# Kernel tuning notes

Measured on AMD Instinct MI355X. Metric: run time of the kernel, lower is better.

The kernel has to match this reference:

```python
import jax, jax.numpy as jnp
import numpy as np

B, T, C = 4, 2048, 1024
HEAD = 2048

def setup_inputs() -> dict:
    key = jax.random.key(0)
    ks = jax.random.split(key, 7)
    s = 1.0 / np.sqrt(C)
    return {
        "x":  jax.random.normal(ks[0], (B, T, C), dtype=jnp.float32),
        "Wq": jax.random.uniform(ks[1], (C, HEAD), dtype=jnp.float32, minval=-s, maxval=s),
        "bq": jax.random.uniform(ks[2], (HEAD,), dtype=jnp.float32, minval=-s, maxval=s),
        "Wk": jax.random.uniform(ks[3], (C, HEAD), dtype=jnp.float32, minval=-s, maxval=s),
        "bk": jax.random.uniform(ks[4], (HEAD,), dtype=jnp.float32, minval=-s, maxval=s),
        "Wv": jax.random.uniform(ks[5], (C, HEAD), dtype=jnp.float32, minval=-s, maxval=s),
        "bv": jax.random.uniform(ks[6], (HEAD,), dtype=jnp.float32, minval=-s, maxval=s),
    }

def reference(x, Wq, bq, Wk, bk, Wv, bv):
    # q,k,v: [B,T,HEAD]
    q = jnp.einsum('btc,ch->bth', x, Wq) + bq
    k = jnp.einsum('btc,ch->bth', x, Wk) + bk
    v = jnp.einsum('btc,ch->bth', x, Wv) + bv
    scale = x.shape[-1] ** -0.5  # NOTE: original scales by n_embed**-0.5, not head_size
    wei = jnp.einsum('bth,bsh->bts', q, k) * scale  # [B,T,T]
    Tn = x.shape[1]
    causal = jnp.tril(jnp.ones((Tn, Tn), dtype=bool))
    wei = jnp.where(causal, wei, -jnp.inf)
    wei = jax.nn.softmax(wei, axis=-1)
    # dropout is identity in eval mode
    out = jnp.einsum('bts,bsh->bth', wei, v)  # [B,T,HEAD]
    return out
```

## Files before the change

### kernel.cpp

```cpp
#include <hip/hip_runtime.h>


#define T_    2048
#define C_    1024
#define B_    4
#define NQK   4096
#define SCALE 0.03125f

typedef __attribute__((ext_vector_type(4))) float floatx4;
typedef __attribute__((ext_vector_type(8))) short short8;
typedef __attribute__((ext_vector_type(8))) unsigned short ushortx8;

__device__ __forceinline__ unsigned short f2bf(float f) {
  unsigned int u = __float_as_uint(f);
  unsigned int r = (u + 0x7fffu + ((u >> 16) & 1u)) >> 16;
  return (unsigned short)r;
}

__global__ void cast_x_kernel(const float* __restrict__ x, ushort* __restrict__ xbf) {
  int i = blockIdx.x * 256 + threadIdx.x;
  float4 v = ((const float4*)x)[i];
  ushort4 o;
  o.x = f2bf(v.x); o.y = f2bf(v.y); o.z = f2bf(v.z); o.w = f2bf(v.w);
  ((ushort4*)xbf)[i] = o;
}

__global__ void wcast_t_kernel(const float* __restrict__ Wq, const float* __restrict__ Wk,
                               const float* __restrict__ Wv, ushort* __restrict__ WtT) {
  int k0 = blockIdx.x * 32;
  int n0 = blockIdx.y * 32;
  const float* W = (n0 < 2048) ? Wq : (n0 < 4096 ? Wk : Wv);
  int nl0 = n0 & 2047;
  __shared__ ushort tile[32][33];
  int tx = threadIdx.x, ty = threadIdx.y;
  for (int r = ty; r < 32; r += 8)
    tile[r][tx] = f2bf(W[(size_t)(k0 + r) * 2048 + nl0 + tx]);
  __syncthreads();
  for (int r = ty; r < 32; r += 8)
    WtT[(size_t)(n0 + r) * 1024 + k0 + tx] = tile[tx][r];
}

__global__ void bias_cat_kernel(const float* __restrict__ bq, const float* __restrict__ bk,
                                const float* __restrict__ bv, float* __restrict__ bcat) {
  int i = blockIdx.x * 256 + threadIdx.x;
  if (i < 6144) {
    const float* s = (i < 2048) ? bq : (i < 4096 ? bk : bv);
    bcat[i] = s[i & 2047];
  }
}

__device__ __forceinline__ void stage128x32(const ushort* g, int ld, char* lds,
                                            int wave, int lane) {
#pragma unroll
  for (int c = 0; c < 2; ++c) {
    int chunk = wave + 4 * c;
    const ushort* gaddr = g + (size_t)(chunk * 16 + (lane >> 2)) * ld + (lane & 3) * 8;
    char* laddr = lds + chunk * 1024;
    __builtin_amdgcn_global_load_lds((const __attribute__((address_space(1))) unsigned int*)gaddr,
                                     (__attribute__((address_space(3))) unsigned int*)laddr,
                                     16, 0, 0);
  }
}

__device__ __forceinline__ void gemm_core(const ushort* A, int lda,
                                          const ushort* Bm, int ldb, int ksteps,
                                          char* ldsA, char* ldsB, floatx4 acc[4][4]) {
  int tid = threadIdx.x;
  int wave = tid >> 6, lane = tid & 63;
  int wm = wave >> 1, wn = wave & 1;
  int koff2 = ((lane >> 4) * 8) * 2;
  int rbase = lane & 15;
  for (int s = 0; s < ksteps; ++s) {
    __syncthreads();
    stage128x32(A + s * 32, lda, ldsA, wave, lane);
    stage128x32(Bm + s * 32, ldb, ldsB, wave, lane);
    __syncthreads();
    short8 af[4], bf[4];
#pragma unroll
    for (int i = 0; i < 4; ++i) {
      af[i] = *(const short8*)(ldsA + (wm * 64 + i * 16 + rbase) * 64 + koff2);
      bf[i] = *(const short8*)(ldsB + (wn * 64 + i * 16 + rbase) * 64 + koff2);
    }
#pragma unroll
    for (int i = 0; i < 4; ++i)
#pragma unroll
      for (int j = 0; j < 4; ++j)
        acc[i][j] = __builtin_amdgcn_mfma_f32_16x16x32_bf16(af[i], bf[j], acc[i][j], 0, 0, 0);
  }
}


#define MFMA16(a, b, c) __builtin_amdgcn_mfma_f32_16x16x32_bf16((a), (b), (c), 0, 0, 0)

#define GLDS16(gsrc, ldst)                                                                       \
  __builtin_amdgcn_global_load_lds((const __attribute__((address_space(1))) unsigned int*)(gsrc), \
                                   (__attribute__((address_space(3))) unsigned int*)(ldst), 16, 0, 0)

template <int LD>
__device__ __forceinline__ void stage_half(const ushort* gsrc, char* ldst) {
  GLDS16(gsrc, ldst);
  GLDS16(gsrc + 8 * LD, ldst + 1024);
}

#define BARX() do {                                        \
  __builtin_amdgcn_sched_barrier(0);                       \
  __builtin_amdgcn_s_barrier();                            \
  __builtin_amdgcn_sched_barrier(0);                       \
} while (0)

template <int LDA, int LDB>
__device__ __forceinline__ void prologue256(const ushort* Ap, const ushort* Bp,
                                            char* lds, int wave, int srcOffA, int srcOffB) {
  stage_half<LDA>(Ap + srcOffA,                     lds + wave * 2048);
  stage_half<LDA>(Ap + 128 * LDA + srcOffA,         lds + 16384 + wave * 2048);
  stage_half<LDB>(Bp + srcOffB,                     lds + 65536 + wave * 2048);
  stage_half<LDB>(Bp + 128 * LDB + srcOffB,         lds + 81920 + wave * 2048);
  stage_half<LDB>(Bp + 64 + srcOffB,                lds + 98304 + wave * 2048);
  stage_half<LDB>(Bp + 64 + 128 * LDB + srcOffB,    lds + 114688 + wave * 2048);
  __builtin_amdgcn_sched_barrier(0);
  asm volatile("s_waitcnt vmcnt(4)" ::: "memory");
  BARX();
}

template <int LDA, int LDB, bool TAIL>
__device__ __forceinline__ void iter256(const ushort* __restrict__ Ap,
                                        const ushort* __restrict__ Bp,
                                        char* lds, int kt0, int wave, int wm, int wn,
                                        int srcOffA, int srcOffB, int lnoff0,
                                        floatx4 (&acc)[8][4]) {
  char* rA0 = lds + wm * 16384;
  char* rA1 = rA0 + 32768;
  char* rB0 = lds + 65536 + (wn >> 1) * 16384 + (wn & 1) * 8192;
  char* rB1 = rB0 + 32768;
  const ushort* sA1 = Ap + (kt0 + 1) * 64 + srcOffA;
  const ushort* sA2 = Ap + (kt0 + 2) * 64 + srcOffA;
  const ushort* sB2 = Bp + (kt0 + 2) * 64 + srcOffB;
  const ushort* sB3 = Bp + (kt0 + 3) * 64 + srcOffB;
  const int lnoff1 = lnoff0 ^ 64;
  short8 af[4][2], b4[4][2];

#pragma unroll
  for (int mi = 0; mi < 4; ++mi) {
    af[mi][0] = *(const short8*)(rA0 + mi * 2048 + lnoff0);
    af[mi][1] = *(const short8*)(rA0 + mi * 2048 + lnoff1);
  }
#pragma unroll
  for (int nj = 0; nj < 4; ++nj) {
    b4[nj][0] = *(const short8*)(rB0 + nj * 2048 + lnoff0);
    b4[nj][1] = *(const short8*)(rB0 + nj * 2048 + lnoff1);
  }
  stage_half<LDA>(sA1, lds + 32768 + wave * 2048);
  stage_half<LDA>(sA1 + 128 * LDA, lds + 49152 + wave * 2048);
  __builtin_amdgcn_s_setprio(1);
#pragma unroll
  for (int mi = 0; mi < 4; ++mi)
#pragma unroll
    for (int nj = 0; nj < 4; ++nj) {
      acc[mi][nj] = MFMA16(af[mi][0], b4[nj][0], acc[mi][nj]);
      acc[mi][nj] = MFMA16(af[mi][1], b4[nj][1], acc[mi][nj]);
    }
  __builtin_amdgcn_s_setprio(0);
  BARX();

#pragma unroll
  for (int mi = 0; mi < 4; ++mi) {
    af[mi][0] = *(const short8*)(rA0 + (4 + mi) * 2048 + lnoff0);
    af[mi][1] = *(const short8*)(rA0 + (4 + mi) * 2048 + lnoff1);
  }
  if constexpr (!TAIL) {
    stage_half<LDB>(sB2, lds + 65536 + wave * 2048);
    stage_half<LDB>(sB2 + 128 * LDB, lds + 81920 + wave * 2048);
  }
  __builtin_amdgcn_s_setprio(1);
#pragma unroll
  for (int mi = 0; mi < 4; ++mi)
#pragma unroll
    for (int nj = 0; nj < 4; ++nj) {
      acc[4 + mi][nj] = MFMA16(af[mi][0], b4[nj][0], acc[4 + mi][nj]);
      acc[4 + mi][nj] = MFMA16(af[mi][1], b4[nj][1], acc[4 + mi][nj]);
    }
  __builtin_amdgcn_s_setprio(0);
  __builtin_amdgcn_sched_barrier(0);
  if constexpr (TAIL) asm volatile("s_waitcnt vmcnt(0)" ::: "memory");
  else                asm volatile("s_waitcnt vmcnt(4)" ::: "memory");
  BARX();

#pragma unroll
  for (int mi = 0; mi < 4; ++mi) {
    af[mi][0] = *(const short8*)(rA1 + mi * 2048 + lnoff0);
    af[mi][1] = *(const short8*)(rA1 + mi * 2048 + lnoff1);
  }
#pragma unroll
  for (int nj = 0; nj < 4; ++nj) {
    b4[nj][0] = *(const short8*)(rB1 + nj * 2048 + lnoff0);
    b4[nj][1] = *(const short8*)(rB1 + nj * 2048 + lnoff1);
  }
  if constexpr (!TAIL) {
    stage_half<LDA>(sA2, lds + wave * 2048);
    stage_half<LDA>(sA2 + 128 * LDA, lds + 16384 + wave * 2048);
  }
  __builtin_amdgcn_s_setprio(1);
#pragma unroll
  for (int mi = 0; mi < 4; ++mi)
#pragma unroll
    for (int nj = 0; nj < 4; ++nj) {
      acc[mi][nj] = MFMA16(af[mi][0], b4[nj][0], acc[mi][nj]);
      acc[mi][nj] = MFMA16(af[mi][1], b4[nj][1], acc[mi][nj]);
    }
  __builtin_amdgcn_s_setprio(0);
  BARX();

#pragma unroll
  for (int mi = 0; mi < 4; ++mi) {
    af[mi][0] = *(const short8*)(rA1 + (4 + mi) * 2048 + lnoff0);
    af[mi][1] = *(const short8*)(rA1 + (4 + mi) * 2048 + lnoff1);
  }
  if constexpr (!TAIL) {
    stage_half<LDB>(sB3, lds + 98304 + wave * 2048);
    stage_half<LDB>(sB3 + 128 * LDB, lds + 114688 + wave * 2048);
  }
  __builtin_amdgcn_s_setprio(1);
#pragma unroll
  for (int mi = 0; mi < 4; ++mi)
#pragma unroll
    for (int nj = 0; nj < 4; ++nj) {
      acc[4 + mi][nj] = MFMA16(af[mi][0], b4[nj][0], acc[4 + mi][nj]);
      acc[4 + mi][nj] = MFMA16(af[mi][1], b4[nj][1], acc[4 + mi][nj]);
    }
  __builtin_amdgcn_s_setprio(0);
  __builtin_amdgcn_sched_barrier(0);
  if constexpr (!TAIL) asm volatile("s_waitcnt vmcnt(4)" ::: "memory");
  BARX();
}

struct Addr256 {
  int wave, wm, wn, ln, ln15, lnoff0;
};
__device__ __forceinline__ Addr256 addr256() {
  Addr256 a;
  int tid = threadIdx.x;
  a.wave = tid >> 6; a.ln = tid & 63;
  a.wm = a.wave >> 2; a.wn = a.wave & 3;
  a.ln15 = a.ln & 15;
  a.lnoff0 = a.ln15 * 128 + (((a.ln >> 4) * 16) ^ ((a.ln15 & 7) << 4));
  return a;
}
template <int LD>
__device__ __forceinline__ int srcOff256(int wave, int ln) {
  return (wave * 16 + (ln >> 3)) * LD + (((ln & 7) * 8) ^ ((ln >> 3) << 3));
}

__global__ __launch_bounds__(512) void gemm_qk256(const ushort* __restrict__ xbf,
                                                  const ushort* __restrict__ WtT,
                                                  const float* __restrict__ bcat,
                                                  ushort* __restrict__ QK) {
  __shared__ __align__(16) char lds[131072];
  int tm = blockIdx.x, tn = blockIdx.y;
  Addr256 a = addr256();
  int srcOff = srcOff256<1024>(a.wave, a.ln);
  const ushort* Ap = xbf + (size_t)tm * 256 * 1024;
  const ushort* Bp = WtT + (size_t)tn * 256 * 1024;
  floatx4 acc[8][4];
#pragma unroll
  for (int i = 0; i < 8; ++i)
#pragma unroll
    for (int j = 0; j < 4; ++j) acc[i][j] = (floatx4){0.f, 0.f, 0.f, 0.f};

  prologue256<1024, 1024>(Ap, Bp, lds, a.wave, srcOff, srcOff);
#pragma unroll 1
  for (int i = 0; i < 7; ++i)
    iter256<1024, 1024, false>(Ap, Bp, lds, 2 * i, a.wave, a.wm, a.wn, srcOff, srcOff, a.lnoff0, acc);
  iter256<1024, 1024, true>(Ap, Bp, lds, 14, a.wave, a.wm, a.wn, srcOff, srcOff, a.lnoff0, acc);

  int colb = a.ln15, rowq = (a.ln >> 4) * 4;
  int colbase = tn * 256 + a.wn * 64 + colb;
  float bias[4];
#pragma unroll
  for (int nj = 0; nj < 4; ++nj) bias[nj] = bcat[colbase + nj * 16];
#pragma unroll
  for (int mi = 0; mi < 8; ++mi) {
    int row = tm * 256 + a.wm * 128 + mi * 16 + rowq;
#pragma unroll
    for (int r = 0; r < 4; ++r) {
      ushort* qrow = QK + (size_t)(row + r) * NQK;
#pragma unroll
      for (int nj = 0; nj < 4; ++nj)
        qrow[colbase + nj * 16] = f2bf(acc[mi][nj][r] + bias[nj]);
    }
  }
}

__global__ __launch_bounds__(512) void gemm_s256(const ushort* __restrict__ QK,
                                                 float* __restrict__ S) {
  int l = blockIdx.x, b = blockIdx.y;
  int tm = (int)((sqrtf(8.f * l + 1.f) - 1.f) * 0.5f);
  while ((tm + 1) * (tm + 2) / 2 <= l) ++tm;
  while (tm * (tm + 1) / 2 > l) --tm;
  int tn = l - tm * (tm + 1) / 2;
  __shared__ __align__(16) char lds[131072];
  Addr256 a = addr256();
  int srcOff = srcOff256<NQK>(a.wave, a.ln);
  const ushort* Ap = QK + (size_t)b * T_ * NQK + (size_t)tm * 256 * NQK;
  const ushort* Bp = QK + (size_t)b * T_ * NQK + (size_t)tn * 256 * NQK + 2048;
  floatx4 acc[8][4];
#pragma unroll
  for (int i = 0; i < 8; ++i)
#pragma unroll
    for (int j = 0; j < 4; ++j) acc[i][j] = (floatx4){0.f, 0.f, 0.f, 0.f};

  prologue256<NQK, NQK>(Ap, Bp, lds, a.wave, srcOff, srcOff);
#pragma unroll 1
  for (int i = 0; i < 15; ++i)
    iter256<NQK, NQK, false>(Ap, Bp, lds, 2 * i, a.wave, a.wm, a.wn, srcOff, srcOff, a.lnoff0, acc);
  iter256<NQK, NQK, true>(Ap, Bp, lds, 30, a.wave, a.wm, a.wn, srcOff, srcOff, a.lnoff0, acc);

  float* Sb = S + (size_t)b * T_ * T_;
  int colb = a.ln15, rowq = (a.ln >> 4) * 4;
  int colbase = tn * 256 + a.wn * 64 + colb;
#pragma unroll
  for (int mi = 0; mi < 8; ++mi) {
    int row = tm * 256 + a.wm * 128 + mi * 16 + rowq;
#pragma unroll
    for (int r = 0; r < 4; ++r) {
      float* srow = Sb + (size_t)(row + r) * T_;
#pragma unroll
      for (int nj = 0; nj < 4; ++nj)
        srow[colbase + nj * 16] = acc[mi][nj][r] * SCALE;
    }
  }
}

__global__ __launch_bounds__(512) void gemm_o256(const ushort* __restrict__ P,
                                                 const ushort* __restrict__ Vt,
                                                 float* __restrict__ O) {
  int tn = blockIdx.x, tm = 7 - blockIdx.y, b = blockIdx.z;
  __shared__ __align__(16) char lds[131072];
  Addr256 a = addr256();
  int srcOff = srcOff256<T_>(a.wave, a.ln);
  const ushort* Ap = P + (size_t)b * T_ * T_ + (size_t)tm * 256 * T_;
  const ushort* Bp = Vt + (size_t)b * T_ * T_ + (size_t)tn * 256 * T_;
  floatx4 acc[8][4];
#pragma unroll
  for (int i = 0; i < 8; ++i)
#pragma unroll
    for (int j = 0; j < 4; ++j) acc[i][j] = (floatx4){0.f, 0.f, 0.f, 0.f};

  int niter = (tm + 1) * 2;
  prologue256<T_, T_>(Ap, Bp, lds, a.wave, srcOff, srcOff);
#pragma unroll 1
  for (int i = 0; i < niter - 1; ++i)
    iter256<T_, T_, false>(Ap, Bp, lds, 2 * i, a.wave, a.wm, a.wn, srcOff, srcOff, a.lnoff0, acc);
  iter256<T_, T_, true>(Ap, Bp, lds, 2 * (niter - 1), a.wave, a.wm, a.wn, srcOff, srcOff, a.lnoff0, acc);

  float* Ob = O + (size_t)b * T_ * T_;
  int colb = a.ln15, rowq = (a.ln >> 4) * 4;
  int colbase = tn * 256 + a.wn * 64 + colb;
#pragma unroll
  for (int mi = 0; mi < 8; ++mi) {
    int row = tm * 256 + a.wm * 128 + mi * 16 + rowq;
#pragma unroll
    for (int r = 0; r < 4; ++r) {
      float* orow = Ob + (size_t)(row + r) * T_;
#pragma unroll
      for (int nj = 0; nj < 4; ++nj)
        orow[colbase + nj * 16] = acc[mi][nj][r];
    }
  }
}

__global__ __launch_bounds__(256) void gemm_v(const ushort* __restrict__ xbf,
                                              const ushort* __restrict__ WtT,
                                              const float* __restrict__ bcat,
                                              ushort* __restrict__ Vt) {
  __shared__ __align__(16) char lds[128 * 136 * 2];
  char* ldsA = lds;
  char* ldsB = lds + 8192;
  int tm = blockIdx.x, tn = blockIdx.y;
  floatx4 acc[4][4];
#pragma unroll
  for (int i = 0; i < 4; ++i)
#pragma unroll
    for (int j = 0; j < 4; ++j) acc[i][j] = (floatx4){0.f, 0.f, 0.f, 0.f};
  gemm_core(xbf + (size_t)tm * 128 * C_, C_, WtT + (size_t)(32 + tn) * 128 * C_, C_,
            C_ / 32, ldsA, ldsB, acc);
  int tid = threadIdx.x, wave = tid >> 6, lane = tid & 63;
  int wm = wave >> 1, wn = wave & 1;
  int colb = lane & 15, rowq = (lane >> 4) * 4;
  __syncthreads();
  ushort* tileT = (ushort*)lds;
#pragma unroll
  for (int j = 0; j < 4; ++j) {
    int h = wn * 64 + j * 16 + colb;
    float bv = bcat[4096 + tn * 128 + h];
#pragma unroll
    for (int i = 0; i < 4; ++i) {
      int s = wm * 64 + i * 16 + rowq;
      ushort4 o4;
      o4.x = f2bf(acc[i][j][0] + bv);
      o4.y = f2bf(acc[i][j][1] + bv);
      o4.z = f2bf(acc[i][j][2] + bv);
      o4.w = f2bf(acc[i][j][3] + bv);
      *(ushort4*)(tileT + h * 136 + s) = o4;
    }
  }
  __syncthreads();
  int b = tm >> 4, sbase = (tm & 15) * 128;
  int hr = tid >> 4, sc = (tid & 15) * 8;
#pragma unroll
  for (int it = 0; it < 8; ++it) {
    int h = it * 16 + hr;
    ushortx8 v = *(const ushortx8*)(tileT + h * 136 + sc);
    *(ushortx8*)(Vt + ((size_t)b * T_ + tn * 128 + h) * T_ + sbase + sc) = v;
  }
}

__global__ __launch_bounds__(256) void softmax_causal(const float* __restrict__ S,
                                                      ushort* __restrict__ P) {
  int t = blockIdx.x, b = blockIdx.y;
  int tid = threadIdx.x;
  const float* srow = S + ((size_t)b * T_ + t) * T_;
  ushort* prow = P + ((size_t)b * T_ + t) * T_;
  int band = ((t >> 8) + 1) << 8;
  float xv[8];
  float m = -INFINITY;
#pragma unroll
  for (int c = 0; c < 2; ++c) {
    int s0 = c * 1024 + tid * 4;
    float* xs = xv + c * 4;
    if (s0 < band) {
      float4 v = *(const float4*)(srow + s0);
      xs[0] = (s0 + 0 <= t) ? v.x : -INFINITY;
      xs[1] = (s0 + 1 <= t) ? v.y : -INFINITY;
      xs[2] = (s0 + 2 <= t) ? v.z : -INFINITY;
      xs[3] = (s0 + 3 <= t) ? v.w : -INFINITY;
      m = fmaxf(fmaxf(fmaxf(xs[0], xs[1]), fmaxf(xs[2], xs[3])), m);
    } else {
      xs[0] = xs[1] = xs[2] = xs[3] = -INFINITY;
    }
  }
  __shared__ float sm4[4];
  int wid = tid >> 6, ln = tid & 63;
#pragma unroll
  for (int o = 32; o; o >>= 1) m = fmaxf(m, __shfl_xor(m, o));
  if (ln == 0) sm4[wid] = m;
  __syncthreads();
  m = fmaxf(fmaxf(sm4[0], sm4[1]), fmaxf(sm4[2], sm4[3]));
  __syncthreads();
  float sum = 0.f;
#pragma unroll
  for (int k = 0; k < 8; ++k) { xv[k] = __expf(xv[k] - m); sum += xv[k]; }
#pragma unroll
  for (int o = 32; o; o >>= 1) sum += __shfl_xor(sum, o);
  if (ln == 0) sm4[wid] = sum;
  __syncthreads();
  sum = sm4[0] + sm4[1] + sm4[2] + sm4[3];
  float inv = 1.0f / sum;
#pragma unroll
  for (int c = 0; c < 2; ++c) {
    int s0 = c * 1024 + tid * 4;
    if (s0 < band) {
      ushort4 o4;
      o4.x = f2bf(xv[c * 4 + 0] * inv);
      o4.y = f2bf(xv[c * 4 + 1] * inv);
      o4.z = f2bf(xv[c * 4 + 2] * inv);
      o4.w = f2bf(xv[c * 4 + 3] * inv);
      *(ushort4*)(prow + s0) = o4;
    }
  }
}

extern "C" void kernel_launch(void* const* d_in, const int* in_sizes, int n_in,
                              void* d_out, int out_size, void* d_ws, size_t ws_size,
                              hipStream_t stream) {
  (void)in_sizes; (void)n_in; (void)out_size; (void)ws_size;
  const float* x  = (const float*)d_in[0];
  const float* Wq = (const float*)d_in[1];
  const float* bq = (const float*)d_in[2];
  const float* Wk = (const float*)d_in[3];
  const float* bk = (const float*)d_in[4];
  const float* Wv = (const float*)d_in[5];
  const float* bv = (const float*)d_in[6];

  char* ws = (char*)d_ws;
  ushort* xbf  = (ushort*)(ws + 0);
  ushort* WtT  = (ushort*)(ws + 16777216);
  float*  bcat = (float*) (ws + 29360128);
  ushort* QK   = (ushort*)(ws + 29384704);
  ushort* P    = (ushort*)(ws + 96493568);
  ushort* Vt   = (ushort*)(ws + 130048000);

  float* S = (float*)d_out;
  float* O = (float*)d_out;

  cast_x_kernel  <<<8192, 256, 0, stream>>>(x, xbf);
  wcast_t_kernel <<<dim3(32, 192), dim3(32, 8), 0, stream>>>(Wq, Wk, Wv, WtT);
  bias_cat_kernel<<<24, 256, 0, stream>>>(bq, bk, bv, bcat);
  gemm_qk256     <<<dim3(32, 16), 512, 0, stream>>>(xbf, WtT, bcat, QK);
  gemm_v         <<<dim3(64, 16), 256, 0, stream>>>(xbf, WtT, bcat, Vt);
  gemm_s256      <<<dim3(36, 4), 512, 0, stream>>>(QK, S);
  softmax_causal <<<dim3(2048, 4), 256, 0, stream>>>(S, P);
  gemm_o256      <<<dim3(8, 8, 4), 512, 0, stream>>>(P, Vt, O);
}
```

Measured before the change: 349.6 us.

## Merge V projection into score GEMM launch with 256-tile pipelined path

Replaces the separate small-tile gemm_v kernel and the gemm_s256 kernel with one launch of 400 blocks. The first 144 blocks compute the causal score tiles and the remaining 256 blocks compute the V projection using the 256x256 pipelined GEMM path, transposing through XOR-swizzled LDS. This fills the GPU better, since the 144-block score grid alone underused it, and it moves V onto the faster pipelined tile code. The cost is heavier per-block work and possible imbalance, because score blocks run twice as many k-steps as V blocks.

```diff
diff --git a/kernel.cpp b/kernel.cpp
--- a/kernel.cpp
+++ b/kernel.cpp
@@ -46,46 +46,6 @@
   if (i < 6144) {
     const float* s = (i < 2048) ? bq : (i < 4096 ? bk : bv);
     bcat[i] = s[i & 2047];
-  }
-}
-
-__device__ __forceinline__ void stage128x32(const ushort* g, int ld, char* lds,
-                                            int wave, int lane) {
-#pragma unroll
-  for (int c = 0; c < 2; ++c) {
-    int chunk = wave + 4 * c;
-    const ushort* gaddr = g + (size_t)(chunk * 16 + (lane >> 2)) * ld + (lane & 3) * 8;
-    char* laddr = lds + chunk * 1024;
-    __builtin_amdgcn_global_load_lds((const __attribute__((address_space(1))) unsigned int*)gaddr,
-                                     (__attribute__((address_space(3))) unsigned int*)laddr,
-                                     16, 0, 0);
-  }
-}
-
-__device__ __forceinline__ void gemm_core(const ushort* A, int lda,
-                                          const ushort* Bm, int ldb, int ksteps,
-                                          char* ldsA, char* ldsB, floatx4 acc[4][4]) {
-  int tid = threadIdx.x;
-  int wave = tid >> 6, lane = tid & 63;
-  int wm = wave >> 1, wn = wave & 1;
-  int koff2 = ((lane >> 4) * 8) * 2;
-  int rbase = lane & 15;
-  for (int s = 0; s < ksteps; ++s) {
-    __syncthreads();
-    stage128x32(A + s * 32, lda, ldsA, wave, lane);
-    stage128x32(Bm + s * 32, ldb, ldsB, wave, lane);
-    __syncthreads();
-    short8 af[4], bf[4];
-#pragma unroll
-    for (int i = 0; i < 4; ++i) {
-      af[i] = *(const short8*)(ldsA + (wm * 64 + i * 16 + rbase) * 64 + koff2);
-      bf[i] = *(const short8*)(ldsB + (wn * 64 + i * 16 + rbase) * 64 + koff2);
-    }
-#pragma unroll
-    for (int i = 0; i < 4; ++i)
-#pragma unroll
-      for (int j = 0; j < 4; ++j)
-        acc[i][j] = __builtin_amdgcn_mfma_f32_16x16x32_bf16(af[i], bf[j], acc[i][j], 0, 0, 0);
   }
 }
 
@@ -290,42 +250,88 @@
   }
 }
 
-__global__ __launch_bounds__(512) void gemm_s256(const ushort* __restrict__ QK,
-                                                 float* __restrict__ S) {
-  int l = blockIdx.x, b = blockIdx.y;
-  int tm = (int)((sqrtf(8.f * l + 1.f) - 1.f) * 0.5f);
-  while ((tm + 1) * (tm + 2) / 2 <= l) ++tm;
-  while (tm * (tm + 1) / 2 > l) --tm;
-  int tn = l - tm * (tm + 1) / 2;
+__global__ __launch_bounds__(512) void gemm_sv(const ushort* __restrict__ QK,
+                                               const ushort* __restrict__ xbf,
+                                               const ushort* __restrict__ WtT,
+                                               const float* __restrict__ bcat,
+                                               float* __restrict__ S,
+                                               ushort* __restrict__ Vt) {
   __shared__ __align__(16) char lds[131072];
+  int l = blockIdx.x;
   Addr256 a = addr256();
-  int srcOff = srcOff256<NQK>(a.wave, a.ln);
-  const ushort* Ap = QK + (size_t)b * T_ * NQK + (size_t)tm * 256 * NQK;
-  const ushort* Bp = QK + (size_t)b * T_ * NQK + (size_t)tn * 256 * NQK + 2048;
   floatx4 acc[8][4];
 #pragma unroll
   for (int i = 0; i < 8; ++i)
 #pragma unroll
     for (int j = 0; j < 4; ++j) acc[i][j] = (floatx4){0.f, 0.f, 0.f, 0.f};
 
-  prologue256<NQK, NQK>(Ap, Bp, lds, a.wave, srcOff, srcOff);
+  if (l < 144) {
+    int t = l % 36, b = l / 36;
+    int tm = (int)((sqrtf(8.f * t + 1.f) - 1.f) * 0.5f);
+    while ((tm + 1) * (tm + 2) / 2 <= t) ++tm;
+    while (tm * (tm + 1) / 2 > t) --tm;
+    int tn = t - tm * (tm + 1) / 2;
+    int srcOff = srcOff256<NQK>(a.wave, a.ln);
+    const ushort* Ap = QK + (size_t)b * T_ * NQK + (size_t)tm * 256 * NQK;
+    const ushort* Bp = QK + (size_t)b * T_ * NQK + (size_t)tn * 256 * NQK + 2048;
+    prologue256<NQK, NQK>(Ap, Bp, lds, a.wave, srcOff, srcOff);
 #pragma unroll 1
-  for (int i = 0; i < 15; ++i)
-    iter256<NQK, NQK, false>(Ap, Bp, lds, 2 * i, a.wave, a.wm, a.wn, srcOff, srcOff, a.lnoff0, acc);
-  iter256<NQK, NQK, true>(Ap, Bp, lds, 30, a.wave, a.wm, a.wn, srcOff, srcOff, a.lnoff0, acc);
-
-  float* Sb = S + (size_t)b * T_ * T_;
-  int colb = a.ln15, rowq = (a.ln >> 4) * 4;
-  int colbase = tn * 256 + a.wn * 64 + colb;
-#pragma unroll
-  for (int mi = 0; mi < 8; ++mi) {
-    int row = tm * 256 + a.wm * 128 + mi * 16 + rowq;
-#pragma unroll
-    for (int r = 0; r < 4; ++r) {
-      float* srow = Sb + (size_t)(row + r) * T_;
-#pragma unroll
-      for (int nj = 0; nj < 4; ++nj)
-        srow[colbase + nj * 16] = acc[mi][nj][r] * SCALE;
+    for (int i = 0; i < 15; ++i)
+      iter256<NQK, NQK, false>(Ap, Bp, lds, 2 * i, a.wave, a.wm, a.wn, srcOff, srcOff, a.lnoff0, acc);
+    iter256<NQK, NQK, true>(Ap, Bp, lds, 30, a.wave, a.wm, a.wn, srcOff, srcOff, a.lnoff0, acc);
+
+    float* Sb = S + (size_t)b * T_ * T_;
+    int colb = a.ln15, rowq = (a.ln >> 4) * 4;
+    int colbase = tn * 256 + a.wn * 64 + colb;
+#pragma unroll
+    for (int mi = 0; mi < 8; ++mi) {
+      int row = tm * 256 + a.wm * 128 + mi * 16 + rowq;
+#pragma unroll
+      for (int r = 0; r < 4; ++r) {
+        float* srow = Sb + (size_t)(row + r) * T_;
+#pragma unroll
+        for (int nj = 0; nj < 4; ++nj)
+          srow[colbase + nj * 16] = acc[mi][nj][r] * SCALE;
+      }
+    }
+  } else {
+    int v = l - 144;
+    int tn = v & 7, tmv = v >> 3;
+    int srcOff = srcOff256<1024>(a.wave, a.ln);
+    const ushort* Ap = xbf + (size_t)tmv * 256 * 1024;
+    const ushort* Bp = WtT + (size_t)(4096 + tn * 256) * 1024;
+    prologue256<1024, 1024>(Ap, Bp, lds, a.wave, srcOff, srcOff);
+#pragma unroll 1
+    for (int i = 0; i < 7; ++i)
+      iter256<1024, 1024, false>(Ap, Bp, lds, 2 * i, a.wave, a.wm, a.wn, srcOff, srcOff, a.lnoff0, acc);
+    iter256<1024, 1024, true>(Ap, Bp, lds, 14, a.wave, a.wm, a.wn, srcOff, srcOff, a.lnoff0, acc);
+
+#pragma unroll
+    for (int nj = 0; nj < 4; ++nj) {
+      int h = a.wn * 64 + nj * 16 + a.ln15;
+      float bv = bcat[4096 + tn * 256 + h];
+      int xr = (h & 31) << 4;
+#pragma unroll
+      for (int mi = 0; mi < 8; ++mi) {
+        int s0 = a.wm * 128 + mi * 16 + (a.ln >> 4) * 4;
+        ushort4 o4;
+        o4.x = f2bf(acc[mi][nj][0] + bv);
+        o4.y = f2bf(acc[mi][nj][1] + bv);
+        o4.z = f2bf(acc[mi][nj][2] + bv);
+        o4.w = f2bf(acc[mi][nj][3] + bv);
+        *(ushort4*)(lds + h * 512 + ((s0 * 2) ^ xr)) = o4;
+      }
+    }
+    __syncthreads();
+    int tid = threadIdx.x;
+    int b = tmv >> 3, sbase = (tmv & 7) * 256;
+    int hr = tid >> 5;
+    int sc16 = tid & 31;
+#pragma unroll
+    for (int it = 0; it < 16; ++it) {
+      int h = it * 16 + hr;
+      ushortx8 vv = *(const ushortx8*)(lds + h * 512 + ((sc16 * 16) ^ ((h & 31) << 4)));
+      *(ushortx8*)(Vt + ((size_t)b * T_ + tn * 256 + h) * T_ + sbase + sc16 * 8) = vv;
     }
   }
 }
@@ -365,52 +371,6 @@
       for (int nj = 0; nj < 4; ++nj)
         orow[colbase + nj * 16] = acc[mi][nj][r];
     }
-  }
-}
-
-__global__ __launch_bounds__(256) void gemm_v(const ushort* __restrict__ xbf,
-                                              const ushort* __restrict__ WtT,
-                                              const float* __restrict__ bcat,
-                                              ushort* __restrict__ Vt) {
-  __shared__ __align__(16) char lds[128 * 136 * 2];
-  char* ldsA = lds;
-  char* ldsB = lds + 8192;
-  int tm = blockIdx.x, tn = blockIdx.y;
-  floatx4 acc[4][4];
-#pragma unroll
-  for (int i = 0; i < 4; ++i)
-#pragma unroll
-    for (int j = 0; j < 4; ++j) acc[i][j] = (floatx4){0.f, 0.f, 0.f, 0.f};
-  gemm_core(xbf + (size_t)tm * 128 * C_, C_, WtT + (size_t)(32 + tn) * 128 * C_, C_,
-            C_ / 32, ldsA, ldsB, acc);
-  int tid = threadIdx.x, wave = tid >> 6, lane = tid & 63;
-  int wm = wave >> 1, wn = wave & 1;
-  int colb = lane & 15, rowq = (lane >> 4) * 4;
-  __syncthreads();
-  ushort* tileT = (ushort*)lds;
-#pragma unroll
-  for (int j = 0; j < 4; ++j) {
-    int h = wn * 64 + j * 16 + colb;
-    float bv = bcat[4096 + tn * 128 + h];
-#pragma unroll
-    for (int i = 0; i < 4; ++i) {
-      int s = wm * 64 + i * 16 + rowq;
-      ushort4 o4;
-      o4.x = f2bf(acc[i][j][0] + bv);
-      o4.y = f2bf(acc[i][j][1] + bv);
-      o4.z = f2bf(acc[i][j][2] + bv);
-      o4.w = f2bf(acc[i][j][3] + bv);
-      *(ushort4*)(tileT + h * 136 + s) = o4;
-    }
-  }
-  __syncthreads();
-  int b = tm >> 4, sbase = (tm & 15) * 128;
-  int hr = tid >> 4, sc = (tid & 15) * 8;
-#pragma unroll
-  for (int it = 0; it < 8; ++it) {
-    int h = it * 16 + hr;
-    ushortx8 v = *(const ushortx8*)(tileT + h * 136 + sc);
-    *(ushortx8*)(Vt + ((size_t)b * T_ + tn * 128 + h) * T_ + sbase + sc) = v;
   }
 }
 
@@ -496,8 +456,7 @@
   wcast_t_kernel <<<dim3(32, 192), dim3(32, 8), 0, stream>>>(Wq, Wk, Wv, WtT);
   bias_cat_kernel<<<24, 256, 0, stream>>>(bq, bk, bv, bcat);
   gemm_qk256     <<<dim3(32, 16), 512, 0, stream>>>(xbf, WtT, bcat, QK);
-  gemm_v         <<<dim3(64, 16), 256, 0, stream>>>(xbf, WtT, bcat, Vt);
-  gemm_s256      <<<dim3(36, 4), 512, 0, stream>>>(QK, S);
+  gemm_sv        <<<400, 512, 0, stream>>>(QK, xbf, WtT, bcat, S, Vt);
   softmax_causal <<<dim3(2048, 4), 256, 0, stream>>>(S, P);
   gemm_o256      <<<dim3(8, 8, 4), 512, 0, stream>>>(P, Vt, O);
 }
```

Measured after the change: 335.2 us. 1.04x faster.
